# Kernel tuning notes

Hardware: AMD Instinct MI355X
Metric: run time of the kernel (lower is better)

## Reference

```python
import jax, jax.numpy as jnp
import numpy as np

LAMDA = 1.0


def setup_inputs() -> dict:
    key = jax.random.key(0)
    k1, k2, k3, k4 = jax.random.split(key, 4)
    B, C, D = 16384, 1000, 512
    logits = jax.random.normal(k1, (B, C), dtype=jnp.float32)
    labels = jax.random.randint(k2, (B,), 0, C, dtype=jnp.int64)
    features = jax.random.normal(k3, (B, D), dtype=jnp.float32)
    global_protos = jax.random.normal(k4, (C, D), dtype=jnp.float32)
    return {"logits": logits, "labels": labels, "features": features,
            "global_protos": global_protos}


def reference(logits, labels, features, global_protos):
    # --- classification loss: mean cross-entropy ---
    logp = jax.nn.log_softmax(logits, axis=-1)                 # [B, C]
    ce_loss = -jnp.take_along_axis(logp, labels[:, None], axis=1).mean()
    ce_loss = jnp.where(jnp.isfinite(ce_loss), ce_loss, 0.0)

    # --- prototype alignment loss ---
    # Every label has a (finite) global prototype, so the per-sample dict
    # loop reduces to: gather proto by label, per-sample MSE, mean over B.
    gathered = global_protos[labels]                           # [B, D]
    per_sample_mse = jnp.mean((features - gathered) ** 2, axis=-1)  # [B]
    proto_loss = per_sample_mse.mean()

    total_loss = ce_loss + LAMDA * proto_loss
    total_loss = jnp.where(jnp.isfinite(total_loss), total_loss, ce_loss)
    return (total_loss, ce_loss, proto_loss)
```

## Files before the change

### kernel.cpp

```cpp
#include <hip/hip_runtime.h>
#include <math.h>


#ifndef INFINITY
#define INFINITY __builtin_inff()
#endif

__device__ __forceinline__ float safe_exp(float dm) {
    return __expf(fminf(dm, 0.0f));
}

__global__ __launch_bounds__(256) void fedtgp_rows(
    const float* __restrict__ logits,
    const int*   __restrict__ labels,
    const float* __restrict__ features,
    const float* __restrict__ protos,
    float2* __restrict__ part,
    int B, int C, int D)
{
    const int tid  = threadIdx.x;
    const int lane = tid & 63;
    const int wv   = tid >> 6;
    const int row  = blockIdx.x * 4 + wv;
    if (row >= B) return;

    const int lab = labels[row];
    const int C4 = C >> 2;
    const int D4 = D >> 2;
    const float* lrow = logits + (size_t)row * C;

    float ce, pl;

    if (C4 >= 64 && C4 <= 256 && D4 >= 64 && D4 <= 128 &&
        (C & 3) == 0 && (D & 3) == 0) {
        const float4* l4 = (const float4*)lrow;
        const float4* f4 = (const float4*)(features + (size_t)row * D);
        const float4* p4 = (const float4*)(protos   + (size_t)lab * D);

        const int i1 = min(lane + 64,  C4 - 1);
        const int i2 = min(lane + 128, C4 - 1);
        const int i3 = min(lane + 192, C4 - 1);
        const int j1 = min(lane + 64,  D4 - 1);

        float4 v0 = l4[lane];
        float4 v1 = l4[i1];
        float4 v2 = l4[i2];
        float4 v3 = l4[i3];
        float4 f0 = f4[lane];
        float4 f1 = f4[j1];
        float4 p0 = p4[lane];
        float4 p1 = p4[j1];
        const float ll = lrow[lab];

        const bool b1 = (lane + 64  < C4);
        const bool b2 = (lane + 128 < C4);
        const bool b3 = (lane + 192 < C4);
        const bool d1 = (lane + 64  < D4);
        const float NI = -INFINITY;
        v1.x = b1 ? v1.x : NI; v1.y = b1 ? v1.y : NI;
        v1.z = b1 ? v1.z : NI; v1.w = b1 ? v1.w : NI;
        v2.x = b2 ? v2.x : NI; v2.y = b2 ? v2.y : NI;
        v2.z = b2 ? v2.z : NI; v2.w = b2 ? v2.w : NI;
        v3.x = b3 ? v3.x : NI; v3.y = b3 ? v3.y : NI;
        v3.z = b3 ? v3.z : NI; v3.w = b3 ? v3.w : NI;

        float m = fmaxf(fmaxf(fmaxf(v0.x, v0.y), fmaxf(v0.z, v0.w)),
                        fmaxf(fmaxf(v1.x, v1.y), fmaxf(v1.z, v1.w)));
        m = fmaxf(m, fmaxf(fmaxf(v2.x, v2.y), fmaxf(v2.z, v2.w)));
        m = fmaxf(m, fmaxf(fmaxf(v3.x, v3.y), fmaxf(v3.z, v3.w)));

        float s = safe_exp(v0.x - m) + safe_exp(v0.y - m)
                + safe_exp(v0.z - m) + safe_exp(v0.w - m);
        s += safe_exp(v1.x - m) + safe_exp(v1.y - m)
           + safe_exp(v1.z - m) + safe_exp(v1.w - m);
        s += safe_exp(v2.x - m) + safe_exp(v2.y - m)
           + safe_exp(v2.z - m) + safe_exp(v2.w - m);
        s += safe_exp(v3.x - m) + safe_exp(v3.y - m)
           + safe_exp(v3.z - m) + safe_exp(v3.w - m);

        float dx = f0.x - p0.x, dy = f0.y - p0.y;
        float dz = f0.z - p0.z, dw = f0.w - p0.w;
        float q = dx * dx + dy * dy + dz * dz + dw * dw;
        dx = f1.x - p1.x; dy = f1.y - p1.y;
        dz = f1.z - p1.z; dw = f1.w - p1.w;
        float q1 = dx * dx + dy * dy + dz * dz + dw * dw;
        q += d1 ? q1 : 0.0f;

        float M = m;
        #pragma unroll
        for (int off = 32; off > 0; off >>= 1)
            M = fmaxf(M, __shfl_xor(M, off, 64));
        s *= safe_exp(m - M);
        #pragma unroll
        for (int off = 32; off > 0; off >>= 1) {
            s += __shfl_xor(s, off, 64);
            q += __shfl_xor(q, off, 64);
        }

        ce = (M + __logf(s)) - ll;
        pl = q / (float)D;
    } else {
        float m = -INFINITY, s = 0.f, q = 0.f;
        for (int c = lane; c < C; c += 64) {
            const float x  = lrow[c];
            const float cm = fmaxf(m, x);
            s = s * safe_exp(m - cm) + safe_exp(x - cm);
            m = cm;
        }
        for (int d = lane; d < D; d += 64) {
            const float df = features[(size_t)row * D + d]
                           - protos[(size_t)lab * D + d];
            q += df * df;
        }
        const float ll = lrow[lab];
        #pragma unroll
        for (int off = 32; off > 0; off >>= 1) {
            const float om = __shfl_xor(m, off, 64);
            const float os = __shfl_xor(s, off, 64);
            q += __shfl_xor(q, off, 64);
            const float nm = fmaxf(m, om);
            s = s * safe_exp(m - nm) + os * safe_exp(om - nm);
            m = nm;
        }
        ce = (m + __logf(s)) - ll;
        pl = q / (float)D;
    }

    if (lane == 0) part[row] = make_float2(ce, pl);
}

__global__ __launch_bounds__(1024) void fedtgp_finalize(
    const float2* __restrict__ part,
    float* __restrict__ out,
    int B, double invB)
{
    const int tid  = threadIdx.x;
    const int lane = tid & 63;
    const int wv   = tid >> 6;
    __shared__ double rc[16];
    __shared__ double rp[16];

    double c = 0.0, p = 0.0;
    for (int i = tid; i < B; i += 1024) {
        const float2 v = part[i];
        c += (double)v.x;
        p += (double)v.y;
    }
    #pragma unroll
    for (int off = 32; off > 0; off >>= 1) {
        c += __shfl_xor(c, off, 64);
        p += __shfl_xor(p, off, 64);
    }
    if (lane == 0) { rc[wv] = c; rp[wv] = p; }
    __syncthreads();

    if (tid == 0) {
        double cs = 0.0, ps = 0.0;
        #pragma unroll
        for (int k = 0; k < 16; ++k) { cs += rc[k]; ps += rp[k]; }
        float ce = (float)(cs * invB);
        float pl = (float)(ps * invB);
        if (!isfinite(ce)) ce = 0.0f;
        float tot = ce + pl;
        if (!isfinite(tot)) tot = ce;
        out[0] = tot;
        out[1] = ce;
        out[2] = pl;
    }
}

extern "C" void kernel_launch(void* const* d_in, const int* in_sizes, int n_in,
                              void* d_out, int out_size, void* d_ws, size_t ws_size,
                              hipStream_t stream)
{
    const float* logits   = (const float*)d_in[0];
    const int*   labels   = (const int*)  d_in[1];
    const float* features = (const float*)d_in[2];
    const float* protos   = (const float*)d_in[3];
    float* out = (float*)d_out;

    const int B = in_sizes[1];
    const int C = in_sizes[0] / B;
    const int D = in_sizes[2] / B;

    float2* part = (float2*)d_ws;

    const int nb = (B + 3) / 4;
    fedtgp_rows<<<nb, 256, 0, stream>>>(logits, labels, features, protos,
                                        part, B, C, D);
    fedtgp_finalize<<<1, 1024, 0, stream>>>(part, out, B, 1.0 / (double)B);
}
```

Measured before the change: 122.1 us.

## Process four rows per wave with double-buffered register prefetch

Each wavefront now handles four consecutive rows instead of one. Loads for the next row are issued into a second register buffer while the current row's softmax and MSE reductions run, so memory latency overlaps with compute. The grid is a quarter of its former size, which lowers block count and launch parallelism but raises register pressure and could reduce occupancy.

```diff
diff --git a/kernel.cpp b/kernel.cpp
--- a/kernel.cpp
+++ b/kernel.cpp
@@ -9,6 +9,8 @@
 __device__ __forceinline__ float safe_exp(float dm) {
     return __expf(fminf(dm, 0.0f));
 }
+
+#define RPW 4
 
 __global__ __launch_bounds__(256) void fedtgp_rows(
     const float* __restrict__ logits,
@@ -21,112 +23,139 @@
     const int tid  = threadIdx.x;
     const int lane = tid & 63;
     const int wv   = tid >> 6;
-    const int row  = blockIdx.x * 4 + wv;
-    if (row >= B) return;
-
-    const int lab = labels[row];
+    const int wave = blockIdx.x * 4 + wv;
+    const int base = wave * RPW;
+    if (base >= B) return;
+
     const int C4 = C >> 2;
     const int D4 = D >> 2;
-    const float* lrow = logits + (size_t)row * C;
-
-    float ce, pl;
-
-    if (C4 >= 64 && C4 <= 256 && D4 >= 64 && D4 <= 128 &&
-        (C & 3) == 0 && (D & 3) == 0) {
-        const float4* l4 = (const float4*)lrow;
-        const float4* f4 = (const float4*)(features + (size_t)row * D);
-        const float4* p4 = (const float4*)(protos   + (size_t)lab * D);
+
+    const bool fast = (base + RPW <= B) &&
+                      (C4 >= 64 && C4 <= 256 && D4 >= 64 && D4 <= 128 &&
+                       (C & 3) == 0 && (D & 3) == 0);
+
+    if (fast) {
+        int labs[RPW];
+        #pragma unroll
+        for (int r = 0; r < RPW; ++r) labs[r] = labels[base + r];
+
+        float4 v[2][4], f[2][2], p[2][2];
+        float ll[RPW];
 
         const int i1 = min(lane + 64,  C4 - 1);
         const int i2 = min(lane + 128, C4 - 1);
         const int i3 = min(lane + 192, C4 - 1);
         const int j1 = min(lane + 64,  D4 - 1);
-
-        float4 v0 = l4[lane];
-        float4 v1 = l4[i1];
-        float4 v2 = l4[i2];
-        float4 v3 = l4[i3];
-        float4 f0 = f4[lane];
-        float4 f1 = f4[j1];
-        float4 p0 = p4[lane];
-        float4 p1 = p4[j1];
-        const float ll = lrow[lab];
-
         const bool b1 = (lane + 64  < C4);
         const bool b2 = (lane + 128 < C4);
         const bool b3 = (lane + 192 < C4);
         const bool d1 = (lane + 64  < D4);
-        const float NI = -INFINITY;
-        v1.x = b1 ? v1.x : NI; v1.y = b1 ? v1.y : NI;
-        v1.z = b1 ? v1.z : NI; v1.w = b1 ? v1.w : NI;
-        v2.x = b2 ? v2.x : NI; v2.y = b2 ? v2.y : NI;
-        v2.z = b2 ? v2.z : NI; v2.w = b2 ? v2.w : NI;
-        v3.x = b3 ? v3.x : NI; v3.y = b3 ? v3.y : NI;
-        v3.z = b3 ? v3.z : NI; v3.w = b3 ? v3.w : NI;
-
-        float m = fmaxf(fmaxf(fmaxf(v0.x, v0.y), fmaxf(v0.z, v0.w)),
-                        fmaxf(fmaxf(v1.x, v1.y), fmaxf(v1.z, v1.w)));
-        m = fmaxf(m, fmaxf(fmaxf(v2.x, v2.y), fmaxf(v2.z, v2.w)));
-        m = fmaxf(m, fmaxf(fmaxf(v3.x, v3.y), fmaxf(v3.z, v3.w)));
-
-        float s = safe_exp(v0.x - m) + safe_exp(v0.y - m)
-                + safe_exp(v0.z - m) + safe_exp(v0.w - m);
-        s += safe_exp(v1.x - m) + safe_exp(v1.y - m)
-           + safe_exp(v1.z - m) + safe_exp(v1.w - m);
-        s += safe_exp(v2.x - m) + safe_exp(v2.y - m)
-           + safe_exp(v2.z - m) + safe_exp(v2.w - m);
-        s += safe_exp(v3.x - m) + safe_exp(v3.y - m)
-           + safe_exp(v3.z - m) + safe_exp(v3.w - m);
-
-        float dx = f0.x - p0.x, dy = f0.y - p0.y;
-        float dz = f0.z - p0.z, dw = f0.w - p0.w;
-        float q = dx * dx + dy * dy + dz * dz + dw * dw;
-        dx = f1.x - p1.x; dy = f1.y - p1.y;
-        dz = f1.z - p1.z; dw = f1.w - p1.w;
-        float q1 = dx * dx + dy * dy + dz * dz + dw * dw;
-        q += d1 ? q1 : 0.0f;
-
-        float M = m;
-        #pragma unroll
-        for (int off = 32; off > 0; off >>= 1)
-            M = fmaxf(M, __shfl_xor(M, off, 64));
-        s *= safe_exp(m - M);
-        #pragma unroll
-        for (int off = 32; off > 0; off >>= 1) {
-            s += __shfl_xor(s, off, 64);
-            q += __shfl_xor(q, off, 64);
+
+#define ISSUE(BUF, RR)                                                        \
+        {                                                                     \
+            const int row_ = base + (RR);                                     \
+            const float* lrow_ = logits + (size_t)row_ * C;                   \
+            const float4* l4_ = (const float4*)lrow_;                         \
+            const float4* f4_ = (const float4*)(features + (size_t)row_ * D); \
+            const float4* p4_ = (const float4*)(protos + (size_t)labs[RR] * D);\
+            v[BUF][0] = l4_[lane];                                            \
+            v[BUF][1] = l4_[i1];                                              \
+            v[BUF][2] = l4_[i2];                                              \
+            v[BUF][3] = l4_[i3];                                              \
+            f[BUF][0] = f4_[lane];  f[BUF][1] = f4_[j1];                      \
+            p[BUF][0] = p4_[lane];  p[BUF][1] = p4_[j1];                      \
+            ll[RR] = lrow_[labs[RR]];                                         \
         }
 
-        ce = (M + __logf(s)) - ll;
-        pl = q / (float)D;
+#define COMPUTE(BUF, RR)                                                      \
+        {                                                                     \
+            const float NI = -INFINITY;                                       \
+            float4 w1 = v[BUF][1], w2 = v[BUF][2], w3 = v[BUF][3];            \
+            w1.x = b1 ? w1.x : NI; w1.y = b1 ? w1.y : NI;                     \
+            w1.z = b1 ? w1.z : NI; w1.w = b1 ? w1.w : NI;                     \
+            w2.x = b2 ? w2.x : NI; w2.y = b2 ? w2.y : NI;                     \
+            w2.z = b2 ? w2.z : NI; w2.w = b2 ? w2.w : NI;                     \
+            w3.x = b3 ? w3.x : NI; w3.y = b3 ? w3.y : NI;                     \
+            w3.z = b3 ? w3.z : NI; w3.w = b3 ? w3.w : NI;                     \
+            const float4 w0 = v[BUF][0];                                      \
+            float m = fmaxf(fmaxf(fmaxf(w0.x, w0.y), fmaxf(w0.z, w0.w)),      \
+                            fmaxf(fmaxf(w1.x, w1.y), fmaxf(w1.z, w1.w)));     \
+            m = fmaxf(m, fmaxf(fmaxf(w2.x, w2.y), fmaxf(w2.z, w2.w)));        \
+            m = fmaxf(m, fmaxf(fmaxf(w3.x, w3.y), fmaxf(w3.z, w3.w)));        \
+            float s = safe_exp(w0.x - m) + safe_exp(w0.y - m)                 \
+                    + safe_exp(w0.z - m) + safe_exp(w0.w - m);                \
+            s += safe_exp(w1.x - m) + safe_exp(w1.y - m)                      \
+               + safe_exp(w1.z - m) + safe_exp(w1.w - m);                     \
+            s += safe_exp(w2.x - m) + safe_exp(w2.y - m)                      \
+               + safe_exp(w2.z - m) + safe_exp(w2.w - m);                     \
+            s += safe_exp(w3.x - m) + safe_exp(w3.y - m)                      \
+               + safe_exp(w3.z - m) + safe_exp(w3.w - m);                     \
+            float dx = f[BUF][0].x - p[BUF][0].x;                             \
+            float dy = f[BUF][0].y - p[BUF][0].y;                             \
+            float dz = f[BUF][0].z - p[BUF][0].z;                             \
+            float dw = f[BUF][0].w - p[BUF][0].w;                             \
+            float q = dx*dx + dy*dy + dz*dz + dw*dw;                          \
+            dx = f[BUF][1].x - p[BUF][1].x; dy = f[BUF][1].y - p[BUF][1].y;   \
+            dz = f[BUF][1].z - p[BUF][1].z; dw = f[BUF][1].w - p[BUF][1].w;   \
+            const float q1 = dx*dx + dy*dy + dz*dz + dw*dw;                   \
+            q += d1 ? q1 : 0.0f;                                              \
+            float M = m;                                                      \
+            _Pragma("unroll")                                                 \
+            for (int off = 32; off > 0; off >>= 1)                            \
+                M = fmaxf(M, __shfl_xor(M, off, 64));                         \
+            s *= safe_exp(m - M);                                             \
+            _Pragma("unroll")                                                 \
+            for (int off = 32; off > 0; off >>= 1) {                          \
+                s += __shfl_xor(s, off, 64);                                  \
+                q += __shfl_xor(q, off, 64);                                  \
+            }                                                                 \
+            if (lane == 0)                                                    \
+                part[base + (RR)] = make_float2((M + __logf(s)) - ll[RR],     \
+                                                q / (float)D);                \
+        }
+
+        ISSUE(0, 0);
+        ISSUE(1, 1);
+        COMPUTE(0, 0);
+        ISSUE(0, 2);
+        COMPUTE(1, 1);
+        ISSUE(1, 3);
+        COMPUTE(0, 2);
+        COMPUTE(1, 3);
+#undef ISSUE
+#undef COMPUTE
     } else {
-        float m = -INFINITY, s = 0.f, q = 0.f;
-        for (int c = lane; c < C; c += 64) {
-            const float x  = lrow[c];
-            const float cm = fmaxf(m, x);
-            s = s * safe_exp(m - cm) + safe_exp(x - cm);
-            m = cm;
+        for (int r = 0; r < RPW; ++r) {
+            const int row = base + r;
+            if (row >= B) break;
+            const int lab = labels[row];
+            const float* lrow = logits + (size_t)row * C;
+            float m = -INFINITY, s = 0.f, q = 0.f;
+            for (int c = lane; c < C; c += 64) {
+                const float x  = lrow[c];
+                const float cm = fmaxf(m, x);
+                s = s * safe_exp(m - cm) + safe_exp(x - cm);
+                m = cm;
+            }
+            for (int d = lane; d < D; d += 64) {
+                const float df = features[(size_t)row * D + d]
+                               - protos[(size_t)lab * D + d];
+                q += df * df;
+            }
+            const float ll2 = lrow[lab];
+            #pragma unroll
+            for (int off = 32; off > 0; off >>= 1) {
+                const float om = __shfl_xor(m, off, 64);
+                const float os = __shfl_xor(s, off, 64);
+                q += __shfl_xor(q, off, 64);
+                const float nm = fmaxf(m, om);
+                s = s * safe_exp(m - nm) + os * safe_exp(om - nm);
+                m = nm;
+            }
+            if (lane == 0)
+                part[row] = make_float2((m + __logf(s)) - ll2, q / (float)D);
         }
-        for (int d = lane; d < D; d += 64) {
-            const float df = features[(size_t)row * D + d]
-                           - protos[(size_t)lab * D + d];
-            q += df * df;
-        }
-        const float ll = lrow[lab];
-        #pragma unroll
-        for (int off = 32; off > 0; off >>= 1) {
-            const float om = __shfl_xor(m, off, 64);
-            const float os = __shfl_xor(s, off, 64);
-            q += __shfl_xor(q, off, 64);
-            const float nm = fmaxf(m, om);
-            s = s * safe_exp(m - nm) + os * safe_exp(om - nm);
-            m = nm;
-        }
-        ce = (m + __logf(s)) - ll;
-        pl = q / (float)D;
-    }
-
-    if (lane == 0) part[row] = make_float2(ce, pl);
+    }
 }
 
 __global__ __launch_bounds__(1024) void fedtgp_finalize(
@@ -185,7 +214,8 @@
 
     float2* part = (float2*)d_ws;
 
-    const int nb = (B + 3) / 4;
+    const int waves = (B + RPW - 1) / RPW;
+    const int nb = (waves + 3) / 4;
     fedtgp_rows<<<nb, 256, 0, stream>>>(logits, labels, features, protos,
                                         part, B, C, D);
     fedtgp_finalize<<<1, 1024, 0, stream>>>(part, out, B, 1.0 / (double)B);
```

New measurement: 125.0 us. +2.3%, slower.

## Split CE and prototype-MSE work into separate blocks with nontemporal loads

Applied to the files above, without the earlier changes.

Work is now split by block role. Four blocks of every five compute cross-entropy for one row per wave. The fifth block computes the prototype MSE for four rows per wave, double-buffering its feature and prototype loads. Streamed logits and features use nontemporal loads to avoid polluting cache, so the reused prototypes stay resident. Partial results move to separate CE and PL arrays. The aim is better memory-level parallelism and cache behaviour, at the cost of more complex indexing and a fast path restricted to D=512 and B divisible by 16.

```diff
diff --git a/kernel.cpp b/kernel.cpp
--- a/kernel.cpp
+++ b/kernel.cpp
@@ -6,8 +6,15 @@
 #define INFINITY __builtin_inff()
 #endif
 
+typedef float float4n __attribute__((ext_vector_type(4)));
+
 __device__ __forceinline__ float safe_exp(float dm) {
     return __expf(fminf(dm, 0.0f));
+}
+
+__device__ __forceinline__ float4 ntload(const float4* p) {
+    const float4n v = __builtin_nontemporal_load((const float4n*)p);
+    return make_float4(v.x, v.y, v.z, v.w);
 }
 
 __global__ __launch_bounds__(256) void fedtgp_rows(
@@ -15,122 +22,170 @@
     const int*   __restrict__ labels,
     const float* __restrict__ features,
     const float* __restrict__ protos,
-    float2* __restrict__ part,
+    float* __restrict__ part_ce,
+    float* __restrict__ part_pl,
     int B, int C, int D)
 {
     const int tid  = threadIdx.x;
     const int lane = tid & 63;
     const int wv   = tid >> 6;
-    const int row  = blockIdx.x * 4 + wv;
-    if (row >= B) return;
-
-    const int lab = labels[row];
     const int C4 = C >> 2;
     const int D4 = D >> 2;
-    const float* lrow = logits + (size_t)row * C;
-
-    float ce, pl;
-
-    if (C4 >= 64 && C4 <= 256 && D4 >= 64 && D4 <= 128 &&
-        (C & 3) == 0 && (D & 3) == 0) {
-        const float4* l4 = (const float4*)lrow;
-        const float4* f4 = (const float4*)(features + (size_t)row * D);
-        const float4* p4 = (const float4*)(protos   + (size_t)lab * D);
-
-        const int i1 = min(lane + 64,  C4 - 1);
-        const int i2 = min(lane + 128, C4 - 1);
-        const int i3 = min(lane + 192, C4 - 1);
-        const int j1 = min(lane + 64,  D4 - 1);
-
-        float4 v0 = l4[lane];
-        float4 v1 = l4[i1];
-        float4 v2 = l4[i2];
-        float4 v3 = l4[i3];
-        float4 f0 = f4[lane];
-        float4 f1 = f4[j1];
-        float4 p0 = p4[lane];
-        float4 p1 = p4[j1];
-        const float ll = lrow[lab];
-
-        const bool b1 = (lane + 64  < C4);
-        const bool b2 = (lane + 128 < C4);
-        const bool b3 = (lane + 192 < C4);
-        const bool d1 = (lane + 64  < D4);
-        const float NI = -INFINITY;
-        v1.x = b1 ? v1.x : NI; v1.y = b1 ? v1.y : NI;
-        v1.z = b1 ? v1.z : NI; v1.w = b1 ? v1.w : NI;
-        v2.x = b2 ? v2.x : NI; v2.y = b2 ? v2.y : NI;
-        v2.z = b2 ? v2.z : NI; v2.w = b2 ? v2.w : NI;
-        v3.x = b3 ? v3.x : NI; v3.y = b3 ? v3.y : NI;
-        v3.z = b3 ? v3.z : NI; v3.w = b3 ? v3.w : NI;
-
-        float m = fmaxf(fmaxf(fmaxf(v0.x, v0.y), fmaxf(v0.z, v0.w)),
-                        fmaxf(fmaxf(v1.x, v1.y), fmaxf(v1.z, v1.w)));
-        m = fmaxf(m, fmaxf(fmaxf(v2.x, v2.y), fmaxf(v2.z, v2.w)));
-        m = fmaxf(m, fmaxf(fmaxf(v3.x, v3.y), fmaxf(v3.z, v3.w)));
-
-        float s = safe_exp(v0.x - m) + safe_exp(v0.y - m)
-                + safe_exp(v0.z - m) + safe_exp(v0.w - m);
-        s += safe_exp(v1.x - m) + safe_exp(v1.y - m)
-           + safe_exp(v1.z - m) + safe_exp(v1.w - m);
-        s += safe_exp(v2.x - m) + safe_exp(v2.y - m)
-           + safe_exp(v2.z - m) + safe_exp(v2.w - m);
-        s += safe_exp(v3.x - m) + safe_exp(v3.y - m)
-           + safe_exp(v3.z - m) + safe_exp(v3.w - m);
-
-        float dx = f0.x - p0.x, dy = f0.y - p0.y;
-        float dz = f0.z - p0.z, dw = f0.w - p0.w;
-        float q = dx * dx + dy * dy + dz * dz + dw * dw;
-        dx = f1.x - p1.x; dy = f1.y - p1.y;
-        dz = f1.z - p1.z; dw = f1.w - p1.w;
-        float q1 = dx * dx + dy * dy + dz * dz + dw * dw;
-        q += d1 ? q1 : 0.0f;
-
-        float M = m;
-        #pragma unroll
-        for (int off = 32; off > 0; off >>= 1)
-            M = fmaxf(M, __shfl_xor(M, off, 64));
-        s *= safe_exp(m - M);
-        #pragma unroll
-        for (int off = 32; off > 0; off >>= 1) {
-            s += __shfl_xor(s, off, 64);
-            q += __shfl_xor(q, off, 64);
+
+    const bool fast = (C4 >= 64 && C4 <= 256 && D4 == 128 &&
+                       (C & 3) == 0 && (D & 3) == 0 && (B & 15) == 0);
+
+    if (fast) {
+        const int unit = blockIdx.x / 5;
+        const int slot = blockIdx.x - unit * 5;
+
+        if (slot < 4) {
+            const int row  = (unit * 4 + slot) * 4 + wv;
+            const int lab  = labels[row];
+            const float* lrow = logits + (size_t)row * C;
+            const float4* l4  = (const float4*)lrow;
+
+            const int i1 = min(lane + 64,  C4 - 1);
+            const int i2 = min(lane + 128, C4 - 1);
+            const int i3 = min(lane + 192, C4 - 1);
+
+            float4 v0 = ntload(&l4[lane]);
+            float4 v1 = ntload(&l4[i1]);
+            float4 v2 = ntload(&l4[i2]);
+            float4 v3 = ntload(&l4[i3]);
+            const float ll = lrow[lab];
+
+            const bool b1 = (lane + 64  < C4);
+            const bool b2 = (lane + 128 < C4);
+            const bool b3 = (lane + 192 < C4);
+            const float NI = -INFINITY;
+            v1.x = b1 ? v1.x : NI; v1.y = b1 ? v1.y : NI;
+            v1.z = b1 ? v1.z : NI; v1.w = b1 ? v1.w : NI;
+            v2.x = b2 ? v2.x : NI; v2.y = b2 ? v2.y : NI;
+            v2.z = b2 ? v2.z : NI; v2.w = b2 ? v2.w : NI;
+            v3.x = b3 ? v3.x : NI; v3.y = b3 ? v3.y : NI;
+            v3.z = b3 ? v3.z : NI; v3.w = b3 ? v3.w : NI;
+
+            float m = fmaxf(fmaxf(fmaxf(v0.x, v0.y), fmaxf(v0.z, v0.w)),
+                            fmaxf(fmaxf(v1.x, v1.y), fmaxf(v1.z, v1.w)));
+            m = fmaxf(m, fmaxf(fmaxf(v2.x, v2.y), fmaxf(v2.z, v2.w)));
+            m = fmaxf(m, fmaxf(fmaxf(v3.x, v3.y), fmaxf(v3.z, v3.w)));
+
+            float s = safe_exp(v0.x - m) + safe_exp(v0.y - m)
+                    + safe_exp(v0.z - m) + safe_exp(v0.w - m);
+            s += safe_exp(v1.x - m) + safe_exp(v1.y - m)
+               + safe_exp(v1.z - m) + safe_exp(v1.w - m);
+            s += safe_exp(v2.x - m) + safe_exp(v2.y - m)
+               + safe_exp(v2.z - m) + safe_exp(v2.w - m);
+            s += safe_exp(v3.x - m) + safe_exp(v3.y - m)
+               + safe_exp(v3.z - m) + safe_exp(v3.w - m);
+
+            float M = m;
+            #pragma unroll
+            for (int off = 32; off > 0; off >>= 1)
+                M = fmaxf(M, __shfl_xor(M, off, 64));
+            s *= safe_exp(m - M);
+            #pragma unroll
+            for (int off = 32; off > 0; off >>= 1)
+                s += __shfl_xor(s, off, 64);
+
+            if (lane == 0)
+                part_ce[row] = (M + __logf(s)) - ll;
+        } else {
+            const int base = (unit * 4 + wv) * 4;
+            const int4 lb = *(const int4*)(labels + base);
+            const int l0 = lb.x, l1 = lb.y, l2 = lb.z, l3 = lb.w;
+
+            float4 f[2][2], p[2][2];
+            float q0, q1, q2, q3;
+
+#define MISSUE(BUF, RR, LAB)                                                  \
+            {                                                                 \
+                const float4* f4_ = (const float4*)(features +                \
+                                      (size_t)(base + (RR)) * D);             \
+                const float4* p4_ = (const float4*)(protos +                  \
+                                      (size_t)(LAB) * D);                     \
+                f[BUF][0] = ntload(&f4_[lane]);                               \
+                f[BUF][1] = ntload(&f4_[lane + 64]);                          \
+                p[BUF][0] = p4_[lane];                                        \
+                p[BUF][1] = p4_[lane + 64];                                   \
+            }
+#define MCOMP(BUF, QQ)                                                        \
+            {                                                                 \
+                float dx = f[BUF][0].x - p[BUF][0].x;                         \
+                float dy = f[BUF][0].y - p[BUF][0].y;                         \
+                float dz = f[BUF][0].z - p[BUF][0].z;                         \
+                float dw = f[BUF][0].w - p[BUF][0].w;                         \
+                QQ = dx*dx + dy*dy + dz*dz + dw*dw;                           \
+                dx = f[BUF][1].x - p[BUF][1].x;                               \
+                dy = f[BUF][1].y - p[BUF][1].y;                               \
+                dz = f[BUF][1].z - p[BUF][1].z;                               \
+                dw = f[BUF][1].w - p[BUF][1].w;                               \
+                QQ += dx*dx + dy*dy + dz*dz + dw*dw;                          \
+            }
+            MISSUE(0, 0, l0);
+            MISSUE(1, 1, l1);
+            MCOMP(0, q0);
+            MISSUE(0, 2, l2);
+            MCOMP(1, q1);
+            MISSUE(1, 3, l3);
+            MCOMP(0, q2);
+            MCOMP(1, q3);
+#undef MISSUE
+#undef MCOMP
+
+            #pragma unroll
+            for (int off = 32; off > 0; off >>= 1) {
+                q0 += __shfl_xor(q0, off, 64);
+                q1 += __shfl_xor(q1, off, 64);
+                q2 += __shfl_xor(q2, off, 64);
+                q3 += __shfl_xor(q3, off, 64);
+            }
+            if (lane == 0) {
+                *(float4*)(part_pl + base) =
+                    make_float4(q0 / (float)D, q1 / (float)D,
+                                q2 / (float)D, q3 / (float)D);
+            }
         }
-
-        ce = (M + __logf(s)) - ll;
-        pl = q / (float)D;
     } else {
-        float m = -INFINITY, s = 0.f, q = 0.f;
-        for (int c = lane; c < C; c += 64) {
-            const float x  = lrow[c];
-            const float cm = fmaxf(m, x);
-            s = s * safe_exp(m - cm) + safe_exp(x - cm);
-            m = cm;
+        const int wave_id = blockIdx.x * 4 + wv;
+        const int nwaves  = gridDim.x * 4;
+        for (int row = wave_id; row < B; row += nwaves) {
+            const int lab = labels[row];
+            const float* lrow = logits + (size_t)row * C;
+            float m = -INFINITY, s = 0.f, q = 0.f;
+            for (int c = lane; c < C; c += 64) {
+                const float x  = lrow[c];
+                const float cm = fmaxf(m, x);
+                s = s * safe_exp(m - cm) + safe_exp(x - cm);
+                m = cm;
+            }
+            for (int d = lane; d < D; d += 64) {
+                const float df = features[(size_t)row * D + d]
+                               - protos[(size_t)lab * D + d];
+                q += df * df;
+            }
+            const float ll = lrow[lab];
+            #pragma unroll
+            for (int off = 32; off > 0; off >>= 1) {
+                const float om = __shfl_xor(m, off, 64);
+                const float os = __shfl_xor(s, off, 64);
+                q += __shfl_xor(q, off, 64);
+                const float nm = fmaxf(m, om);
+                s = s * safe_exp(m - nm) + os * safe_exp(om - nm);
+                m = nm;
+            }
+            if (lane == 0) {
+                part_ce[row] = (m + __logf(s)) - ll;
+                part_pl[row] = q / (float)D;
+            }
         }
-        for (int d = lane; d < D; d += 64) {
-            const float df = features[(size_t)row * D + d]
-                           - protos[(size_t)lab * D + d];
-            q += df * df;
-        }
-        const float ll = lrow[lab];
-        #pragma unroll
-        for (int off = 32; off > 0; off >>= 1) {
-            const float om = __shfl_xor(m, off, 64);
-            const float os = __shfl_xor(s, off, 64);
-            q += __shfl_xor(q, off, 64);
-            const float nm = fmaxf(m, om);
-            s = s * safe_exp(m - nm) + os * safe_exp(om - nm);
-            m = nm;
-        }
-        ce = (m + __logf(s)) - ll;
-        pl = q / (float)D;
-    }
-
-    if (lane == 0) part[row] = make_float2(ce, pl);
+    }
 }
 
 __global__ __launch_bounds__(1024) void fedtgp_finalize(
-    const float2* __restrict__ part,
+    const float* __restrict__ part_ce,
+    const float* __restrict__ part_pl,
     float* __restrict__ out,
     int B, double invB)
 {
@@ -142,9 +197,8 @@
 
     double c = 0.0, p = 0.0;
     for (int i = tid; i < B; i += 1024) {
-        const float2 v = part[i];
-        c += (double)v.x;
-        p += (double)v.y;
+        c += (double)part_ce[i];
+        p += (double)part_pl[i];
     }
     #pragma unroll
     for (int off = 32; off > 0; off >>= 1) {
@@ -183,10 +237,18 @@
     const int C = in_sizes[0] / B;
     const int D = in_sizes[2] / B;
 
-    float2* part = (float2*)d_ws;
-
-    const int nb = (B + 3) / 4;
+    const int C4 = C >> 2;
+    const int D4 = D >> 2;
+    const bool fast = (C4 >= 64 && C4 <= 256 && D4 == 128 &&
+                       (C & 3) == 0 && (D & 3) == 0 && (B & 15) == 0);
+
+    float* part_ce = (float*)d_ws;
+    float* part_pl = part_ce + B;
+
+    const int nb = fast ? (B / 16) * 5
+                        : (B + 3) / 4;
     fedtgp_rows<<<nb, 256, 0, stream>>>(logits, labels, features, protos,
-                                        part, B, C, D);
-    fedtgp_finalize<<<1, 1024, 0, stream>>>(part, out, B, 1.0 / (double)B);
-}
+                                        part_ce, part_pl, B, C, D);
+    fedtgp_finalize<<<1, 1024, 0, stream>>>(part_ce, part_pl, out, B,
+                                            1.0 / (double)B);
+}
```

New measurement: 131.7 us. 7.9% more time.
